# Performance work log

Hardware: AMD Instinct MI355X
Metric: run time of the kernel (lower is better)

## Reference

```python
import jax, jax.numpy as jnp
import numpy as np

DT = 1e-6  # system.dt

# kind codes: 0=R, 1=IVS, 2=VC, 3=SW, 4=C, 5=L

def setup_inputs() -> dict:
    E, N, SIG = 2048, 1024, 64
    key = jax.random.key(0)
    k1, k2, k3, k4 = jax.random.split(key, 4)
    M = jax.random.normal(k1, (N, E), dtype=jnp.float32)
    # positive, bounded away from zero (module clamps params to [1e-15, 1e15])
    params = jax.random.uniform(k2, (E,), dtype=jnp.float32, minval=0.5, maxval=1.5)
    sw_params = jax.random.normal(k3, (E, SIG), dtype=jnp.float32)
    kinds = jax.random.randint(k4, (E,), 0, 6, dtype=jnp.int32)
    return {"M": M, "params": params, "sw_params": sw_params, "kinds": kinds, "time": 1}


def _element_vals(params, sw_params, kinds, time):
    # per-element z/y diagonal values, vectorized over all elements
    sw_on = jax.nn.sigmoid(sw_params[:, time]) > 0.5
    one = jnp.ones_like(params)
    zero = jnp.zeros_like(params)
    ndt = -DT / params
    z_vals = jnp.select(
        [kinds == 0, kinds == 1, kinds == 2, kinds == 3, kinds == 4, kinds == 5],
        [-params,    zero,       one,        jnp.where(sw_on, 0.0, 1.0), ndt, one],
    )
    y_vals = jnp.select(
        [kinds == 0, kinds == 1, kinds == 2, kinds == 3, kinds == 4, kinds == 5],
        [one,        one,        zero,       jnp.where(sw_on, 1.0, 0.0), one, ndt],
    )
    return z_vals, y_vals


def reference(M, params, sw_params, kinds, time):
    N, E = M.shape
    z_vals, y_vals = _element_vals(params, sw_params, kinds, time)
    zNE = jnp.zeros((N, E), dtype=M.dtype)
    zNN = jnp.zeros((N, N), dtype=M.dtype)
    zEE = jnp.zeros((E, E), dtype=M.dtype)
    zEN = jnp.zeros((E, N), dtype=M.dtype)
    eye = jnp.eye(E, dtype=M.dtype)
    kcl = jnp.concatenate([M, zNE, zNN], axis=1)            # [N, 2E+N]
    kvl = jnp.concatenate([zEE, eye, -M.T], axis=1)          # [E, 2E+N]
    elem = jnp.concatenate([jnp.diag(z_vals), jnp.diag(y_vals), zEN], axis=1)  # [E, 2E+N]
    return jnp.concatenate([kcl, kvl, elem], axis=0)         # [N+2E, 2E+N]
```

## Files before the change

### kernel.cpp

```cpp
#include <hip/hip_runtime.h>
#include <hip/hip_bf16.h>

#define N_   1024
#define E_   2048
#define W_   (2 * E_ + N_)
#define SIG_ 64
#define ROWS_ (N_ + 2 * E_)

union V8 {
    float  f[8];
    float4 q[2];
};

__global__ __launch_bounds__(256) void coeff_kernel(
    const float* __restrict__ M,
    const float* __restrict__ params,
    const float* __restrict__ sw,
    const int*   __restrict__ kinds,
    const int*   __restrict__ time_p,
    float*       __restrict__ out)
{
    const int idx = blockIdx.x * 256 + threadIdx.x;
    const int row = idx / (W_ / 8);
    const int c0  = (idx - row * (W_ / 8)) * 8;

    V8 v;
#pragma unroll
    for (int j = 0; j < 8; ++j) v.f[j] = 0.0f;

    if (row < N_) {
        if (c0 < E_) {
            v.q[0] = *reinterpret_cast<const float4*>(M + row * E_ + c0);
            v.q[1] = *reinterpret_cast<const float4*>(M + row * E_ + c0 + 4);
        }
    } else if (row < N_ + E_) {
        const int e = row - N_;
        if (c0 >= 2 * E_) {
            const int n0 = c0 - 2 * E_;
#pragma unroll
            for (int j = 0; j < 8; ++j)
                v.f[j] = 0.0f - M[(size_t)(n0 + j) * E_ + e];
        } else {
            const int d = (E_ + e) - c0;
            if (d >= 0 && d < 8) v.f[d] = 1.0f;
        }
    } else {
        const int e  = row - (N_ + E_);
        const int dz = e - c0;
        const int dy = (E_ + e) - c0;
        const bool hz = (dz >= 0) && (dz < 8);
        const bool hy = (dy >= 0) && (dy < 8);
        if (hz || hy) {
            const int   kind = kinds[e];
            const float p    = params[e];

            int t = *time_p;
            if ((unsigned)t >= (unsigned)SIG_) {
                union { int i; float f; } tu; tu.i = t;
                t = (int)tu.f;
                if ((unsigned)t >= (unsigned)SIG_) t = 0;
            }
            const bool  sw_on = sw[e * SIG_ + t] > 0.0f;
            const float ndt   = -1e-6f / p;
            float z, y;
            switch (kind) {
                case 0:  z = -p;                  y = 1.0f;                break;
                case 1:  z = 0.0f;                y = 1.0f;                break;
                case 2:  z = 1.0f;                y = 0.0f;                break;
                case 3:  z = sw_on ? 0.0f : 1.0f; y = sw_on ? 1.0f : 0.0f; break;
                case 4:  z = ndt;                 y = 1.0f;                break;
                default: z = 1.0f;                y = ndt;                 break;
            }
            if (hz) v.f[dz] = z;
            if (hy) v.f[dy] = y;
        }
    }

    float* dst = out + (size_t)row * W_ + c0;
    *reinterpret_cast<float4*>(dst)     = v.q[0];
    *reinterpret_cast<float4*>(dst + 4) = v.q[1];
}

extern "C" void kernel_launch(void* const* d_in, const int* in_sizes, int n_in,
                              void* d_out, int out_size, void* d_ws, size_t ws_size,
                              hipStream_t stream) {
    const float* M      = (const float*)d_in[0];
    const float* params = (const float*)d_in[1];
    const float* sw     = (const float*)d_in[2];
    const int*   kinds  = (const int*)d_in[3];
    const int*   time_p = (const int*)d_in[4];
    float* out          = (float*)d_out;

    const int total_threads = (ROWS_ * W_) / 8;
    const int block = 256;
    const int grid  = total_threads / block;
    coeff_kernel<<<grid, block, 0, stream>>>(M, params, sw, kinds, time_p, out);
}
```

Measured before the change: 151.0 us.

## Transpose -M.T block via shared-memory tiles and use nontemporal stores

The -M.T region was previously built by strided gathers with one scalar load per element. It is now produced by dedicated 64x64 tiled blocks that load M coalesced, stage it in padded LDS and write the transpose coalesced. The remaining regions get their own block ranges with simpler index math. All output writes become nontemporal stores to avoid cache pollution on this write-heavy kernel. The cost is a more complex block dispatch and shared memory allocated in every block.

Result: slower. 159.2 us (+5.5%).

```diff
diff --git a/kernel.cpp b/kernel.cpp
--- a/kernel.cpp
+++ b/kernel.cpp
@@ -1,5 +1,4 @@
 #include <hip/hip_runtime.h>
-#include <hip/hip_bf16.h>
 
 #define N_   1024
 #define E_   2048
@@ -7,9 +6,16 @@
 #define SIG_ 64
 #define ROWS_ (N_ + 2 * E_)
 
+#define TB_  ((E_ / 64) * (N_ / 64))
+#define AB_  ((N_ * (W_ / 8)) / 256)
+#define BB_  ((E_ * (2 * E_ / 8)) / 256)
+#define CB_  ((E_ * (W_ / 8)) / 256)
+
+typedef float vf4 __attribute__((ext_vector_type(4)));
+
 union V8 {
-    float  f[8];
-    float4 q[2];
+    float f[8];
+    vf4   q[2];
 };
 
 __global__ __launch_bounds__(256) void coeff_kernel(
@@ -20,32 +26,67 @@
     const int*   __restrict__ time_p,
     float*       __restrict__ out)
 {
-    const int idx = blockIdx.x * 256 + threadIdx.x;
-    const int row = idx / (W_ / 8);
-    const int c0  = (idx - row * (W_ / 8)) * 8;
+    const int bid = blockIdx.x;
+    const int tid = threadIdx.x;
+
+    __shared__ float tile[64][65];
+
+    if (bid < TB_) {
+        const int e0 = (bid & 31) << 6;
+        const int n0 = (bid >> 5) << 6;
+        const int c4 = (tid & 15) << 2;
+        const int r0 = tid >> 4;
+#pragma unroll
+        for (int k = 0; k < 4; ++k) {
+            const int r = r0 + 16 * k;
+            const vf4 m = *reinterpret_cast<const vf4*>(
+                M + (size_t)(n0 + r) * E_ + e0 + c4);
+            tile[r][c4 + 0] = m.x;
+            tile[r][c4 + 1] = m.y;
+            tile[r][c4 + 2] = m.z;
+            tile[r][c4 + 3] = m.w;
+        }
+        __syncthreads();
+#pragma unroll
+        for (int k = 0; k < 4; ++k) {
+            const int er = r0 + 16 * k;
+            vf4 s;
+            s.x = -tile[c4 + 0][er];
+            s.y = -tile[c4 + 1][er];
+            s.z = -tile[c4 + 2][er];
+            s.w = -tile[c4 + 3][er];
+            float* dst = out + (size_t)(N_ + e0 + er) * W_ + 2 * E_ + n0 + c4;
+            __builtin_nontemporal_store(s, reinterpret_cast<vf4*>(dst));
+        }
+        return;
+    }
 
     V8 v;
 #pragma unroll
     for (int j = 0; j < 8; ++j) v.f[j] = 0.0f;
 
-    if (row < N_) {
+    int row, c0;
+
+    if (bid < TB_ + AB_) {
+        const int u = (bid - TB_) * 256 + tid;
+        row = u / 640;
+        c0  = (u - row * 640) * 8;
         if (c0 < E_) {
-            v.q[0] = *reinterpret_cast<const float4*>(M + row * E_ + c0);
-            v.q[1] = *reinterpret_cast<const float4*>(M + row * E_ + c0 + 4);
+            v.q[0] = *reinterpret_cast<const vf4*>(M + (size_t)row * E_ + c0);
+            v.q[1] = *reinterpret_cast<const vf4*>(M + (size_t)row * E_ + c0 + 4);
         }
-    } else if (row < N_ + E_) {
-        const int e = row - N_;
-        if (c0 >= 2 * E_) {
-            const int n0 = c0 - 2 * E_;
-#pragma unroll
-            for (int j = 0; j < 8; ++j)
-                v.f[j] = 0.0f - M[(size_t)(n0 + j) * E_ + e];
-        } else {
-            const int d = (E_ + e) - c0;
-            if (d >= 0 && d < 8) v.f[d] = 1.0f;
-        }
+    } else if (bid < TB_ + AB_ + BB_) {
+        const int u = (bid - TB_ - AB_) * 256 + tid;
+        const int e = u >> 9;
+        c0  = (u & 511) * 8;
+        row = N_ + e;
+        const int d = (E_ + e) - c0;
+        if (d >= 0 && d < 8) v.f[d] = 1.0f;
     } else {
-        const int e  = row - (N_ + E_);
+        const int u = (bid - TB_ - AB_ - BB_) * 256 + tid;
+        const int e = u / 640;
+        c0  = (u - e * 640) * 8;
+        row = N_ + E_ + e;
         const int dz = e - c0;
         const int dy = (E_ + e) - c0;
         const bool hz = (dz >= 0) && (dz < 8);
@@ -77,8 +118,8 @@
     }
 
     float* dst = out + (size_t)row * W_ + c0;
-    *reinterpret_cast<float4*>(dst)     = v.q[0];
-    *reinterpret_cast<float4*>(dst + 4) = v.q[1];
+    __builtin_nontemporal_store(v.q[0], reinterpret_cast<vf4*>(dst));
+    __builtin_nontemporal_store(v.q[1], reinterpret_cast<vf4*>(dst + 4));
 }
 
 extern "C" void kernel_launch(void* const* d_in, const int* in_sizes, int n_in,
@@ -91,8 +132,7 @@
     const int*   time_p = (const int*)d_in[4];
     float* out          = (float*)d_out;
 
-    const int total_threads = (ROWS_ * W_) / 8;
+    const int grid  = TB_ + AB_ + BB_ + CB_;
     const int block = 256;
-    const int grid  = total_threads / block;
     coeff_kernel<<<grid, block, 0, stream>>>(M, params, sw, kinds, time_p, out);
 }
```
